# Kernel tuning notes

Measured on AMD Instinct MI355X. Metric: run time of the kernel, lower is better.

## Reference

```python
import jax, jax.numpy as jnp
import numpy as np
import jax.scipy.linalg

BATCH = 1048576
M_NUM = 2
DT = 0.0166667
NN_RATIO = 0.5
SLOPE = 0.01  # torch LeakyReLU default negative_slope


def setup_inputs() -> dict:
    key = jax.random.key(0)
    ks = jax.random.split(key, 16)
    inp = {}
    inp["SS"] = jax.random.normal(ks[0], (BATCH, 2), dtype=jnp.float32)
    inp["Alphas"] = jax.random.uniform(ks[1], (BATCH, M_NUM), dtype=jnp.float32)
    # per-muscle scalar parameters (positive so sqrt(K*I) is valid)
    inp["K0s"] = jax.random.uniform(ks[2], (M_NUM,), minval=0.5, maxval=1.5)
    inp["K1s"] = jax.random.uniform(ks[3], (M_NUM,), minval=0.5, maxval=1.5)
    inp["L0s"] = jax.random.uniform(ks[4], (M_NUM,), minval=0.5, maxval=1.5)
    inp["L1s"] = jax.random.uniform(ks[5], (M_NUM,), minval=0.1, maxval=0.6)
    inp["Ms"] = jnp.array([1.0, -1.0], dtype=jnp.float32)  # moment arms
    inp["I_p"] = jnp.array([1.0], dtype=jnp.float32)
    inp["B_p"] = jnp.array([0.05], dtype=jnp.float32)
    inp["K_p"] = jnp.array([1.0], dtype=jnp.float32)
    # per-muscle compensational MLP weights: 3-32-32-32-1 (eval mode, dropout off)
    s = 0.1
    inp["W1"] = jax.random.normal(ks[6], (M_NUM, 3, 32)) * s
    inp["b1"] = jax.random.normal(ks[7], (M_NUM, 32)) * s
    inp["W2"] = jax.random.normal(ks[8], (M_NUM, 32, 32)) * s
    inp["b2"] = jax.random.normal(ks[9], (M_NUM, 32)) * s
    inp["W3"] = jax.random.normal(ks[10], (M_NUM, 32, 32)) * s
    inp["b3"] = jax.random.normal(ks[11], (M_NUM, 32)) * s
    inp["W4"] = jax.random.normal(ks[12], (M_NUM, 32, 1)) * s
    inp["b4"] = jax.random.normal(ks[13], (M_NUM, 1)) * s
    return inp


def _leaky(x):
    return jnp.where(x >= 0, x, SLOPE * x)


def reference(SS, Alphas, K0s, K1s, L0s, L1s, Ms, I_p, B_p, K_p,
              W1, b1, W2, b2, W3, b3, W4, b4):
    B = SS.shape[0]
    a = jnp.clip(Alphas, 0.0, 1.0)                      # (B, m)
    # muscle length / speed via scalar moment arms
    l = SS[:, 0:1] * Ms[None, :]                        # (B, m)
    dl = SS[:, 1:2] * Ms[None, :]                       # (B, m)
    # compensational MLPs, vectorized over muscles
    x = jnp.stack([l, dl, a], axis=-1)                  # (B, m, 3)
    h = _leaky(jnp.einsum('bmi,mio->bmo', x, W1) + b1[None])
    h = _leaky(jnp.einsum('bmi,mio->bmo', h, W2) + b2[None])
    h = _leaky(jnp.einsum('bmi,mio->bmo', h, W3) + b3[None])
    nn_out = jnp.tanh(jnp.einsum('bmi,mio->bmo', h, W4) + b4[None])[..., 0] * NN_RATIO  # (B, m)

    I0, B0p, K0p = I_p[0], B_p[0], K_p[0]
    K_m = K0s[None, :] + K1s[None, :] * a               # (B, m)
    K_tot = jnp.sum(K_m * Ms[None, :] ** 2, axis=1)     # (B,)
    A10 = -(K_tot + K0p) / I0
    D = 2.0 * jnp.sqrt(K_tot * I0)
    A11 = -(D + B0p) / I0
    B_F = K_m * (L0s[None, :] + L1s[None, :] * a - jnp.abs(l)) \
        + K1s[None, :] * L1s[None, :] * a * a * nn_out   # (B, m)
    B10 = jnp.sum(B_F * Ms[None, :], axis=1) / I0       # (B,)

    # Build block matrix M6 = [[A*dt, B*dt, 0], [0, 0, I2], [0, 0, 0]]
    M6 = jnp.zeros((B, 6, 6), dtype=SS.dtype)
    M6 = M6.at[:, 0, 1].set(DT)
    M6 = M6.at[:, 1, 0].set(A10 * DT)
    M6 = M6.at[:, 1, 1].set(A11 * DT)
    M6 = M6.at[:, 1, 2].set(B10 * DT)
    M6 = M6.at[:, 1, 3].set(DT / I0)
    M6 = M6.at[:, 2, 4].set(1.0)
    M6 = M6.at[:, 3, 5].set(1.0)

    expMT = jax.vmap(jax.scipy.linalg.expm)(M6)         # (B, 6, 6)
    Ad = expMT[:, :2, :2]
    Bd1 = expMT[:, :2, 4:6]
    Bd0 = expMT[:, :2, 2:4] - Bd1
    u = jnp.array([1.0, 0.0], dtype=SS.dtype)           # U0 = U1 = [1, 0]
    SSout = (jnp.einsum('bij,bj->bi', Ad, SS)
             + jnp.einsum('bij,j->bi', Bd0, u)
             + jnp.einsum('bij,j->bi', Bd1, u))          # (B, 2)
    return SSout[:, :1], SSout
```

## Files before the change

kernel.cpp:

```cpp
#include <hip/hip_runtime.h>
#include <hip/hip_bf16.h>

#define NTHREADS 256
#define WAVES    4
#define GPW      4
#define DT_F     0.0166667f

typedef _Float16 f16x8 __attribute__((ext_vector_type(8)));
typedef _Float16 f16x4 __attribute__((ext_vector_type(4)));
typedef _Float16 f16x2 __attribute__((ext_vector_type(2)));
typedef float    f32x4 __attribute__((ext_vector_type(4)));

#define BF16_PROBE 0xBF803F80u

#define OW1 0
#define OB1 192
#define OW2 256
#define OB2 2368
#define OW3 2432
#define OB3 4544
#define OW4 4608
#define OB4 4672
#define SMEM_F 4680

__device__ __forceinline__ float leaky(float x) { return fmaxf(x, 0.01f * x); }

__device__ __forceinline__ float tanh_fast(float x) {
    const float xc = fminf(fmaxf(x, -10.0f), 10.0f);
    const float t  = __expf(2.0f * xc);
    return (t - 1.0f) * __builtin_amdgcn_rcpf(t + 1.0f);
}

__device__ __forceinline__ f16x2 pkrtz(float a, float b) {
    return __builtin_bit_cast(f16x2, __builtin_amdgcn_cvt_pkrtz(a, b));
}

__device__ __forceinline__ f16x4 leaky_cvt(const f32x4 D) {
    f16x2 lo = pkrtz(D[0], D[1]);
    f16x2 hi = pkrtz(D[2], D[3]);
    const f16x2 sl = {(_Float16)0.01f, (_Float16)0.01f};
    lo = __builtin_elementwise_max(lo, lo * sl);
    hi = __builtin_elementwise_max(hi, hi * sl);
    return __builtin_shufflevector(lo, hi, 0, 1, 2, 3);
}

__device__ __forceinline__ f16x8 concat8(const f16x4 a, const f16x4 b) {
    return __builtin_shufflevector(a, b, 0, 1, 2, 3, 4, 5, 6, 7);
}

__device__ __forceinline__ void epilogue_math(
    const float* P, float ss0, float ss1, float a0, float a1,
    float nn0, float nn1, float& o0f, float& o1f)
{
    const float K00 = P[0], K01 = P[1], K10 = P[2], K11 = P[3];
    const float L00 = P[4], L01 = P[5], L10 = P[6], L11 = P[7];
    const float Ms0 = P[8], Ms1 = P[9];
    const float I0  = P[10], B0p = P[11], K0p = P[12];

    const float Km0   = fmaf(K10, a0, K00);
    const float Km1   = fmaf(K11, a1, K01);
    const float K_tot = Km0*Ms0*Ms0 + Km1*Ms1*Ms1;
    const float invI  = 1.0f / I0;
    const float A10   = -(K_tot + K0p) * invI;
    const float Dd    = 2.0f * sqrtf(K_tot * I0);
    const float A11   = -(Dd + B0p) * invI;
    const float absl0 = fabsf(ss0 * Ms0);
    const float absl1 = fabsf(ss0 * Ms1);
    const float BF0   = Km0 * (L00 + L10*a0 - absl0) + K10*L10*a0*a0*nn0;
    const float BF1   = Km1 * (L01 + L11*a1 - absl1) + K11*L11*a1*a1*nn1;
    const float B10   = (BF0*Ms0 + BF1*Ms1) * invI;

    const float t01 = DT_F;
    const float t10 = A10 * DT_F;
    const float t11 = A11 * DT_F;

    float p00 = 1.0f/120.0f, p01 = 0.0f, p10 = 0.0f, p11 = 1.0f/120.0f;
    const float coef[4] = {1.0f/24.0f, 1.0f/6.0f, 0.5f, 1.0f};
    #pragma unroll
    for (int j = 0; j < 4; ++j) {
        const float cj  = coef[j];
        const float n00 = p01*t10 + cj;
        const float n01 = p00*t01 + p01*t11;
        const float n10 = p11*t10;
        const float n11 = p10*t01 + p11*t11 + cj;
        p00 = n00; p01 = n01; p10 = n10; p11 = n11;
    }
    const float e00 = 1.0f + t01*p10;
    const float e01 = t01*p11;
    const float e10 = t10*p00 + t11*p10;
    const float e11 = 1.0f + t10*p01 + t11*p11;

    const float cscale = DT_F * B10;
    o0f = fmaf(e00, ss0, fmaf(e01, ss1, p01 * cscale));
    o1f = fmaf(e10, ss0, fmaf(e11, ss1, p11 * cscale));
}

__device__ __forceinline__ float ldb(const __hip_bfloat16* p, int i) {
    return __bfloat162float(p[i]);
}

__device__ void run_bf16_fallback(
    const void* SSv, const void* ALv, const void* K0sv, const void* K1sv,
    const void* L0sv, const void* L1sv, const void* Msv, const void* I_pv,
    const void* B_pv, const void* K_pv, const void* W1v, const void* b1v,
    const void* W2v, const void* b2v, const void* W3v, const void* b3v,
    const void* W4v, const void* b4v, void* outv, int batch)
{
    const __hip_bfloat16* SS = (const __hip_bfloat16*)SSv;
    const __hip_bfloat16* AL = (const __hip_bfloat16*)ALv;
    const __hip_bfloat16* W1 = (const __hip_bfloat16*)W1v;
    const __hip_bfloat16* b1 = (const __hip_bfloat16*)b1v;
    const __hip_bfloat16* W2 = (const __hip_bfloat16*)W2v;
    const __hip_bfloat16* b2 = (const __hip_bfloat16*)b2v;
    const __hip_bfloat16* W3 = (const __hip_bfloat16*)W3v;
    const __hip_bfloat16* b3 = (const __hip_bfloat16*)b3v;
    const __hip_bfloat16* W4 = (const __hip_bfloat16*)W4v;
    const __hip_bfloat16* b4 = (const __hip_bfloat16*)b4v;

    float P[13];
    P[0] = ldb((const __hip_bfloat16*)K0sv, 0); P[1] = ldb((const __hip_bfloat16*)K0sv, 1);
    P[2] = ldb((const __hip_bfloat16*)K1sv, 0); P[3] = ldb((const __hip_bfloat16*)K1sv, 1);
    P[4] = ldb((const __hip_bfloat16*)L0sv, 0); P[5] = ldb((const __hip_bfloat16*)L0sv, 1);
    P[6] = ldb((const __hip_bfloat16*)L1sv, 0); P[7] = ldb((const __hip_bfloat16*)L1sv, 1);
    P[8] = ldb((const __hip_bfloat16*)Msv, 0);  P[9] = ldb((const __hip_bfloat16*)Msv, 1);
    P[10] = ldb((const __hip_bfloat16*)I_pv, 0);
    P[11] = ldb((const __hip_bfloat16*)B_pv, 0);
    P[12] = ldb((const __hip_bfloat16*)K_pv, 0);

    const int stride = gridDim.x * blockDim.x;
    for (int e = blockIdx.x * blockDim.x + threadIdx.x; e < batch; e += stride) {
        const float ss0 = ldb(SS, 2*e), ss1 = ldb(SS, 2*e+1);
        float a0 = fminf(fmaxf(ldb(AL, 2*e),   0.0f), 1.0f);
        float a1 = fminf(fmaxf(ldb(AL, 2*e+1), 0.0f), 1.0f);
        float nn[2];
        #pragma unroll 1
        for (int m = 0; m < 2; ++m) {
            const float am = m ? a1 : a0;
            const float l = ss0 * P[8+m], dl = ss1 * P[8+m];
            float h[32];
            #pragma unroll
            for (int o = 0; o < 32; ++o)
                h[o] = leaky(fmaf(l, ldb(W1, m*96+o),
                             fmaf(dl, ldb(W1, m*96+32+o),
                             fmaf(am, ldb(W1, m*96+64+o), ldb(b1, m*32+o)))));
            float g[32];
            #pragma unroll 1
            for (int oc = 0; oc < 4; ++oc) {
                float acc[8];
                #pragma unroll
                for (int j = 0; j < 8; ++j) acc[j] = ldb(b2, m*32+oc*8+j);
                #pragma unroll
                for (int k = 0; k < 32; ++k) {
                    #pragma unroll
                    for (int j = 0; j < 8; ++j)
                        acc[j] = fmaf(h[k], ldb(W2, m*1024+k*32+oc*8+j), acc[j]);
                }
                #pragma unroll
                for (int j = 0; j < 8; ++j) g[oc*8+j] = leaky(acc[j]);
            }
            float h3[32];
            #pragma unroll 1
            for (int oc = 0; oc < 4; ++oc) {
                float acc[8];
                #pragma unroll
                for (int j = 0; j < 8; ++j) acc[j] = ldb(b3, m*32+oc*8+j);
                #pragma unroll
                for (int k = 0; k < 32; ++k) {
                    #pragma unroll
                    for (int j = 0; j < 8; ++j)
                        acc[j] = fmaf(g[k], ldb(W3, m*1024+k*32+oc*8+j), acc[j]);
                }
                #pragma unroll
                for (int j = 0; j < 8; ++j) h3[oc*8+j] = leaky(acc[j]);
            }
            float acc = ldb(b4, m);
            #pragma unroll
            for (int k = 0; k < 32; ++k) acc = fmaf(h3[k], ldb(W4, m*32+k), acc);
            nn[m] = tanh_fast(acc) * 0.5f;
        }
        float o0f, o1f;
        epilogue_math(P, ss0, ss1, a0, a1, nn[0], nn[1], o0f, o1f);
        __hip_bfloat16* out0 = (__hip_bfloat16*)outv;
        __hip_bfloat162* out1 = (__hip_bfloat162*)(out0 + batch);
        out0[e] = __float2bfloat16(o0f);
        __hip_bfloat162 pr;
        pr.x = __float2bfloat16(o0f);
        pr.y = __float2bfloat16(o1f);
        out1[e] = pr;
    }
}

__global__ __launch_bounds__(NTHREADS) void joint_kernel(
    const void* __restrict__ SSv, const void* __restrict__ ALv,
    const void* __restrict__ K0sv, const void* __restrict__ K1sv,
    const void* __restrict__ L0sv, const void* __restrict__ L1sv,
    const void* __restrict__ Msv,  const void* __restrict__ I_pv,
    const void* __restrict__ B_pv, const void* __restrict__ K_pv,
    const void* __restrict__ W1v,  const void* __restrict__ b1v,
    const void* __restrict__ W2v,  const void* __restrict__ b2v,
    const void* __restrict__ W3v,  const void* __restrict__ b3v,
    const void* __restrict__ W4v,  const void* __restrict__ b4v,
    void* __restrict__ outv, int batch)
{
    const unsigned probe = *(const unsigned*)Msv;
    if (probe == BF16_PROBE) {
        run_bf16_fallback(SSv, ALv, K0sv, K1sv, L0sv, L1sv, Msv, I_pv, B_pv,
                          K_pv, W1v, b1v, W2v, b2v, W3v, b3v, W4v, b4v,
                          outv, batch);
        return;
    }

    const float* SS = (const float*)SSv;
    const float* AL = (const float*)ALv;
    const float* W1 = (const float*)W1v;  const float* b1 = (const float*)b1v;
    const float* W2 = (const float*)W2v;  const float* b2 = (const float*)b2v;
    const float* W3 = (const float*)W3v;  const float* b3 = (const float*)b3v;
    const float* W4 = (const float*)W4v;  const float* b4 = (const float*)b4v;

    const int tid  = threadIdx.x;
    const int wave = tid >> 6;
    const int lane = tid & 63;
    const int n    = lane & 15;
    const int q    = lane >> 4;
    const int gh0  = ((n >> 2) << 3) + (n & 3);

    __shared__ __align__(16) float sm[SMEM_F];
    for (int i = tid; i < 192;  i += NTHREADS) sm[OW1+i] = W1[i];
    for (int i = tid; i < 2048; i += NTHREADS) {
        const int mi = i >> 10, rem = i & 1023, in = rem >> 5, out = rem & 31;
        sm[OW2 + mi*1056 + in*33 + out] = W2[i];
        sm[OW3 + mi*1056 + in*33 + out] = W3[i];
    }
    for (int i = tid; i < 64;   i += NTHREADS) {
        sm[OB1+i] = b1[i]; sm[OB2+i] = b2[i];
        sm[OB3+i] = b3[i]; sm[OW4+i] = W4[i];
    }
    if (tid < 2) sm[OB4+tid] = b4[tid];
    __syncthreads();

    f16x4 A1[2][2];
    #pragma unroll
    for (int mi = 0; mi < 2; ++mi)
        #pragma unroll
        for (int h = 0; h < 2; ++h)
            #pragma unroll
            for (int j = 0; j < 4; ++j) {
                const int k = q*4 + j;
                const int g = gh0 + h*4;
                float v = 0.0f;
                if (k < 3)       v = sm[OW1 + mi*96 + k*32 + g];
                else if (k == 3) v = sm[OB1 + mi*32 + g];
                A1[mi][h][j] = (_Float16)v;
            }
    f16x8 A2[2][2], A3[2][2];
    #pragma unroll
    for (int mi = 0; mi < 2; ++mi)
        #pragma unroll
        for (int h = 0; h < 2; ++h) {
            const int g = gh0 + h*4;
            #pragma unroll
            for (int j = 0; j < 8; ++j) {
                const int in = q*8 + j;
                A2[mi][h][j] = (_Float16)sm[OW2 + mi*1056 + in*33 + g];
                A3[mi][h][j] = (_Float16)sm[OW3 + mi*1056 + in*33 + g];
            }
        }
    f16x8 A4[2];
    #pragma unroll
    for (int mi = 0; mi < 2; ++mi)
        #pragma unroll
        for (int j = 0; j < 8; ++j)
            A4[mi][j] = (_Float16)sm[OW4 + mi*32 + q*8 + j];
    f32x4 Cb2[2][2], Cb3[2][2];
    #pragma unroll
    for (int mi = 0; mi < 2; ++mi)
        #pragma unroll
        for (int h = 0; h < 2; ++h) {
            Cb2[mi][h] = *(const f32x4*)&sm[OB2 + mi*32 + q*8 + h*4];
            Cb3[mi][h] = *(const f32x4*)&sm[OB3 + mi*32 + q*8 + h*4];
        }
    const float b4s0 = sm[OB4], b4s1 = sm[OB4+1];

    float P[13];
    P[0]  = ((const float*)K0sv)[0]; P[1]  = ((const float*)K0sv)[1];
    P[2]  = ((const float*)K1sv)[0]; P[3]  = ((const float*)K1sv)[1];
    P[4]  = ((const float*)L0sv)[0]; P[5]  = ((const float*)L0sv)[1];
    P[6]  = ((const float*)L1sv)[0]; P[7]  = ((const float*)L1sv)[1];
    P[8]  = ((const float*)Msv)[0];  P[9]  = ((const float*)Msv)[1];
    P[10] = ((const float*)I_pv)[0];
    P[11] = ((const float*)B_pv)[0];
    P[12] = ((const float*)K_pv)[0];

    const f32x4 zero = {0.0f, 0.0f, 0.0f, 0.0f};
    const int groupBase = (blockIdx.x * WAVES + wave) * GPW;

    #pragma unroll 1
    for (int g = 0; g < GPW; ++g) {
        const int ebase = (groupBase + g) * 64;
        float my_r0 = 0.0f, my_r1 = 0.0f;

        #pragma unroll 1
        for (int p = 0; p < 2; ++p) {
            float2 s[2];
            float a0c[2], a1c[2];
            #pragma unroll
            for (int ti = 0; ti < 2; ++ti) {
                const int e  = ebase + (2*p + ti)*16 + n;
                const int eg = min(e, batch - 1);
                s[ti] = ((const float2*)SS)[eg];
                const float2 al = ((const float2*)AL)[eg];
                a0c[ti] = fminf(fmaxf(al.x, 0.0f), 1.0f);
                a1c[ti] = fminf(fmaxf(al.y, 0.0f), 1.0f);
            }

            f16x4 B1[2][2];
            #pragma unroll
            for (int ti = 0; ti < 2; ++ti)
                #pragma unroll
                for (int mi = 0; mi < 2; ++mi) {
                    const float Msm = P[8 + mi];
                    const float am  = mi ? a1c[ti] : a0c[ti];
                    const f16x2 blo = pkrtz(s[ti].x * Msm, s[ti].y * Msm);
                    const f16x2 bhi = pkrtz(am, 1.0f);
                    B1[ti][mi] = __builtin_shufflevector(blo, bhi, 0, 1, 2, 3);
                }

            f32x4 D[2][2][2];
            #pragma unroll
            for (int ti = 0; ti < 2; ++ti)
                #pragma unroll
                for (int mi = 0; mi < 2; ++mi) {
                    D[ti][mi][0] = __builtin_amdgcn_mfma_f32_16x16x16f16(A1[mi][0], B1[ti][mi], zero, 0, 0, 0);
                    D[ti][mi][1] = __builtin_amdgcn_mfma_f32_16x16x16f16(A1[mi][1], B1[ti][mi], zero, 0, 0, 0);
                }
            f16x8 Bx[2][2];
            #pragma unroll
            for (int ti = 0; ti < 2; ++ti)
                #pragma unroll
                for (int mi = 0; mi < 2; ++mi)
                    Bx[ti][mi] = concat8(leaky_cvt(D[ti][mi][0]), leaky_cvt(D[ti][mi][1]));

            #pragma unroll
            for (int ti = 0; ti < 2; ++ti)
                #pragma unroll
                for (int mi = 0; mi < 2; ++mi) {
                    D[ti][mi][0] = __builtin_amdgcn_mfma_f32_16x16x32_f16(A2[mi][0], Bx[ti][mi], Cb2[mi][0], 0, 0, 0);
                    D[ti][mi][1] = __builtin_amdgcn_mfma_f32_16x16x32_f16(A2[mi][1], Bx[ti][mi], Cb2[mi][1], 0, 0, 0);
                }
            #pragma unroll
            for (int ti = 0; ti < 2; ++ti)
                #pragma unroll
                for (int mi = 0; mi < 2; ++mi)
                    Bx[ti][mi] = concat8(leaky_cvt(D[ti][mi][0]), leaky_cvt(D[ti][mi][1]));

            #pragma unroll
            for (int ti = 0; ti < 2; ++ti)
                #pragma unroll
                for (int mi = 0; mi < 2; ++mi) {
                    D[ti][mi][0] = __builtin_amdgcn_mfma_f32_16x16x32_f16(A3[mi][0], Bx[ti][mi], Cb3[mi][0], 0, 0, 0);
                    D[ti][mi][1] = __builtin_amdgcn_mfma_f32_16x16x32_f16(A3[mi][1], Bx[ti][mi], Cb3[mi][1], 0, 0, 0);
                }
            #pragma unroll
            for (int ti = 0; ti < 2; ++ti)
                #pragma unroll
                for (int mi = 0; mi < 2; ++mi)
                    Bx[ti][mi] = concat8(leaky_cvt(D[ti][mi][0]), leaky_cvt(D[ti][mi][1]));

            #pragma unroll
            for (int ti = 0; ti < 2; ++ti) {
                const bool own = (q == (2*p + ti));
                #pragma unroll
                for (int mi = 0; mi < 2; ++mi) {
                    f32x4 G = __builtin_amdgcn_mfma_f32_16x16x32_f16(A4[mi], Bx[ti][mi], zero, 0, 0, 0);
                    const float r = G[0] + (mi ? b4s1 : b4s0);
                    if (mi == 0) my_r0 = own ? r : my_r0;
                    else         my_r1 = own ? r : my_r1;
                }
            }
        }

        const int eo  = ebase + lane;
        const int eog = min(eo, batch - 1);
        const float2 se  = ((const float2*)SS)[eog];
        const float2 ale = ((const float2*)AL)[eog];
        const float a0 = fminf(fmaxf(ale.x, 0.0f), 1.0f);
        const float a1 = fminf(fmaxf(ale.y, 0.0f), 1.0f);
        const float nn0 = tanh_fast(my_r0) * 0.5f;
        const float nn1 = tanh_fast(my_r1) * 0.5f;
        float o0f, o1f;
        epilogue_math(P, se.x, se.y, a0, a1, nn0, nn1, o0f, o1f);
        if (eo < batch) {
            ((float*)outv)[eo] = o0f;
            ((float2*)((float*)outv + batch))[eo] = make_float2(o0f, o1f);
        }
    }
}

extern "C" void kernel_launch(void* const* d_in, const int* in_sizes, int n_in,
                              void* d_out, int out_size, void* d_ws, size_t ws_size,
                              hipStream_t stream) {
    const int batch = in_sizes[0] / 2;
    const int elemsPerBlock = 64 * GPW * WAVES;
    const int grid = (batch + elemsPerBlock - 1) / elemsPerBlock;
    joint_kernel<<<grid, NTHREADS, 0, stream>>>(
        d_in[0], d_in[1], d_in[2], d_in[3], d_in[4], d_in[5], d_in[6],
        d_in[7], d_in[8], d_in[9], d_in[10], d_in[11], d_in[12], d_in[13],
        d_in[14], d_in[15], d_in[16], d_in[17], d_out, batch);
}
```

Before: 126.8 us.

## Process all four column tiles per group at once and simplify 2x2 expm epilogue

The per-group loop over two half-groups of two 16-column tiles is replaced by one pass over all four tiles. Each MFMA layer stage now issues twice as many independent instructions, which gives more room to hide MFMA latency. The epilogue's 2x2 Taylor/Horner matrix exponential is reduced to a two-scalar recurrence that exploits the fixed t00=0 structure, cutting ALU work. Launch bounds now declare one block per SM so the larger register footprint fits, at the risk of lower occupancy.

Result: slower. 131.1 us (+3.3%).

```diff
diff --git a/kernel.cpp b/kernel.cpp
--- a/kernel.cpp
+++ b/kernel.cpp
@@ -73,26 +73,22 @@
     const float t01 = DT_F;
     const float t10 = A10 * DT_F;
     const float t11 = A11 * DT_F;
-
-    float p00 = 1.0f/120.0f, p01 = 0.0f, p10 = 0.0f, p11 = 1.0f/120.0f;
+    const float u   = t01 * t10;
+
+    float a = 1.0f/120.0f, b = 0.0f;
     const float coef[4] = {1.0f/24.0f, 1.0f/6.0f, 0.5f, 1.0f};
     #pragma unroll
     for (int j = 0; j < 4; ++j) {
-        const float cj  = coef[j];
-        const float n00 = p01*t10 + cj;
-        const float n01 = p00*t01 + p01*t11;
-        const float n10 = p11*t10;
-        const float n11 = p10*t01 + p11*t11 + cj;
-        p00 = n00; p01 = n01; p10 = n10; p11 = n11;
-    }
-    const float e00 = 1.0f + t01*p10;
-    const float e01 = t01*p11;
-    const float e10 = t10*p00 + t11*p10;
-    const float e11 = 1.0f + t10*p01 + t11*p11;
-
-    const float cscale = DT_F * B10;
-    o0f = fmaf(e00, ss0, fmaf(e01, ss1, p01 * cscale));
-    o1f = fmaf(e10, ss0, fmaf(e11, ss1, p11 * cscale));
+        const float an = fmaf(b, u, coef[j]);
+        const float bn = fmaf(b, t11, a);
+        a = an; b = bn;
+    }
+    const float c   = fmaf(b, t11, a);
+    const float e00 = fmaf(b, u, 1.0f);
+    const float cs  = DT_F * B10;
+
+    o0f = fmaf(e00, ss0, fmaf(c * t01, ss1, cs * (b * t01)));
+    o1f = fmaf(c * t10, ss0, fmaf(fmaf(c, t11, e00), ss1, cs * c));
 }
 
 __device__ __forceinline__ float ldb(const __hip_bfloat16* p, int i) {
@@ -190,7 +186,7 @@
     }
 }
 
-__global__ __launch_bounds__(NTHREADS) void joint_kernel(
+__global__ __launch_bounds__(NTHREADS, 1) void joint_kernel(
     const void* __restrict__ SSv, const void* __restrict__ ALv,
     const void* __restrict__ K0sv, const void* __restrict__ K1sv,
     const void* __restrict__ L0sv, const void* __restrict__ L1sv,
@@ -297,85 +293,82 @@
     #pragma unroll 1
     for (int g = 0; g < GPW; ++g) {
         const int ebase = (groupBase + g) * 64;
+
+        float2 s[4];
+        float a0c[4], a1c[4];
+        #pragma unroll
+        for (int t = 0; t < 4; ++t) {
+            const int e  = ebase + t*16 + n;
+            const int eg = min(e, batch - 1);
+            s[t] = ((const float2*)SS)[eg];
+            const float2 al = ((const float2*)AL)[eg];
+            a0c[t] = fminf(fmaxf(al.x, 0.0f), 1.0f);
+            a1c[t] = fminf(fmaxf(al.y, 0.0f), 1.0f);
+        }
+
+        f16x4 B1[4][2];
+        #pragma unroll
+        for (int t = 0; t < 4; ++t)
+            #pragma unroll
+            for (int mi = 0; mi < 2; ++mi) {
+                const float Msm = P[8 + mi];
+                const float am  = mi ? a1c[t] : a0c[t];
+                const f16x2 blo = pkrtz(s[t].x * Msm, s[t].y * Msm);
+                const f16x2 bhi = pkrtz(am, 1.0f);
+                B1[t][mi] = __builtin_shufflevector(blo, bhi, 0, 1, 2, 3);
+            }
+
+        f32x4 D[4][2][2];
+        #pragma unroll
+        for (int t = 0; t < 4; ++t)
+            #pragma unroll
+            for (int mi = 0; mi < 2; ++mi) {
+                D[t][mi][0] = __builtin_amdgcn_mfma_f32_16x16x16f16(A1[mi][0], B1[t][mi], zero, 0, 0, 0);
+                D[t][mi][1] = __builtin_amdgcn_mfma_f32_16x16x16f16(A1[mi][1], B1[t][mi], zero, 0, 0, 0);
+            }
+        f16x8 Bx[4][2];
+        #pragma unroll
+        for (int t = 0; t < 4; ++t)
+            #pragma unroll
+            for (int mi = 0; mi < 2; ++mi)
+                Bx[t][mi] = concat8(leaky_cvt(D[t][mi][0]), leaky_cvt(D[t][mi][1]));
+
+        #pragma unroll
+        for (int t = 0; t < 4; ++t)
+            #pragma unroll
+            for (int mi = 0; mi < 2; ++mi) {
+                D[t][mi][0] = __builtin_amdgcn_mfma_f32_16x16x32_f16(A2[mi][0], Bx[t][mi], Cb2[mi][0], 0, 0, 0);
+                D[t][mi][1] = __builtin_amdgcn_mfma_f32_16x16x32_f16(A2[mi][1], Bx[t][mi], Cb2[mi][1], 0, 0, 0);
+            }
+        #pragma unroll
+        for (int t = 0; t < 4; ++t)
+            #pragma unroll
+            for (int mi = 0; mi < 2; ++mi)
+                Bx[t][mi] = concat8(leaky_cvt(D[t][mi][0]), leaky_cvt(D[t][mi][1]));
+
+        #pragma unroll
+        for (int t = 0; t < 4; ++t)
+            #pragma unroll
+            for (int mi = 0; mi < 2; ++mi) {
+                D[t][mi][0] = __builtin_amdgcn_mfma_f32_16x16x32_f16(A3[mi][0], Bx[t][mi], Cb3[mi][0], 0, 0, 0);
+                D[t][mi][1] = __builtin_amdgcn_mfma_f32_16x16x32_f16(A3[mi][1], Bx[t][mi], Cb3[mi][1], 0, 0, 0);
+            }
+        #pragma unroll
+        for (int t = 0; t < 4; ++t)
+            #pragma unroll
+            for (int mi = 0; mi < 2; ++mi)
+                Bx[t][mi] = concat8(leaky_cvt(D[t][mi][0]), leaky_cvt(D[t][mi][1]));
+
         float my_r0 = 0.0f, my_r1 = 0.0f;
-
-        #pragma unroll 1
-        for (int p = 0; p < 2; ++p) {
-            float2 s[2];
-            float a0c[2], a1c[2];
-            #pragma unroll
-            for (int ti = 0; ti < 2; ++ti) {
-                const int e  = ebase + (2*p + ti)*16 + n;
-                const int eg = min(e, batch - 1);
-                s[ti] = ((const float2*)SS)[eg];
-                const float2 al = ((const float2*)AL)[eg];
-                a0c[ti] = fminf(fmaxf(al.x, 0.0f), 1.0f);
-                a1c[ti] = fminf(fmaxf(al.y, 0.0f), 1.0f);
-            }
-
-            f16x4 B1[2][2];
-            #pragma unroll
-            for (int ti = 0; ti < 2; ++ti)
-                #pragma unroll
-                for (int mi = 0; mi < 2; ++mi) {
-                    const float Msm = P[8 + mi];
-                    const float am  = mi ? a1c[ti] : a0c[ti];
-                    const f16x2 blo = pkrtz(s[ti].x * Msm, s[ti].y * Msm);
-                    const f16x2 bhi = pkrtz(am, 1.0f);
-                    B1[ti][mi] = __builtin_shufflevector(blo, bhi, 0, 1, 2, 3);
-                }
-
-            f32x4 D[2][2][2];
-            #pragma unroll
-            for (int ti = 0; ti < 2; ++ti)
-                #pragma unroll
-                for (int mi = 0; mi < 2; ++mi) {
-                    D[ti][mi][0] = __builtin_amdgcn_mfma_f32_16x16x16f16(A1[mi][0], B1[ti][mi], zero, 0, 0, 0);
-                    D[ti][mi][1] = __builtin_amdgcn_mfma_f32_16x16x16f16(A1[mi][1], B1[ti][mi], zero, 0, 0, 0);
-                }
-            f16x8 Bx[2][2];
-            #pragma unroll
-            for (int ti = 0; ti < 2; ++ti)
-                #pragma unroll
-                for (int mi = 0; mi < 2; ++mi)
-                    Bx[ti][mi] = concat8(leaky_cvt(D[ti][mi][0]), leaky_cvt(D[ti][mi][1]));
-
-            #pragma unroll
-            for (int ti = 0; ti < 2; ++ti)
-                #pragma unroll
-                for (int mi = 0; mi < 2; ++mi) {
-                    D[ti][mi][0] = __builtin_amdgcn_mfma_f32_16x16x32_f16(A2[mi][0], Bx[ti][mi], Cb2[mi][0], 0, 0, 0);
-                    D[ti][mi][1] = __builtin_amdgcn_mfma_f32_16x16x32_f16(A2[mi][1], Bx[ti][mi], Cb2[mi][1], 0, 0, 0);
-                }
-            #pragma unroll
-            for (int ti = 0; ti < 2; ++ti)
-                #pragma unroll
-                for (int mi = 0; mi < 2; ++mi)
-                    Bx[ti][mi] = concat8(leaky_cvt(D[ti][mi][0]), leaky_cvt(D[ti][mi][1]));
-
-            #pragma unroll
-            for (int ti = 0; ti < 2; ++ti)
-                #pragma unroll
-                for (int mi = 0; mi < 2; ++mi) {
-                    D[ti][mi][0] = __builtin_amdgcn_mfma_f32_16x16x32_f16(A3[mi][0], Bx[ti][mi], Cb3[mi][0], 0, 0, 0);
-                    D[ti][mi][1] = __builtin_amdgcn_mfma_f32_16x16x32_f16(A3[mi][1], Bx[ti][mi], Cb3[mi][1], 0, 0, 0);
-                }
-            #pragma unroll
-            for (int ti = 0; ti < 2; ++ti)
-                #pragma unroll
-                for (int mi = 0; mi < 2; ++mi)
-                    Bx[ti][mi] = concat8(leaky_cvt(D[ti][mi][0]), leaky_cvt(D[ti][mi][1]));
-
-            #pragma unroll
-            for (int ti = 0; ti < 2; ++ti) {
-                const bool own = (q == (2*p + ti));
-                #pragma unroll
-                for (int mi = 0; mi < 2; ++mi) {
-                    f32x4 G = __builtin_amdgcn_mfma_f32_16x16x32_f16(A4[mi], Bx[ti][mi], zero, 0, 0, 0);
-                    const float r = G[0] + (mi ? b4s1 : b4s0);
-                    if (mi == 0) my_r0 = own ? r : my_r0;
-                    else         my_r1 = own ? r : my_r1;
-                }
+        #pragma unroll
+        for (int t = 0; t < 4; ++t) {
+            const bool own = (q == t);
+            #pragma unroll
+            for (int mi = 0; mi < 2; ++mi) {
+                f32x4 G = __builtin_amdgcn_mfma_f32_16x16x32_f16(A4[mi], Bx[t][mi], zero, 0, 0, 0);
+                const float r = G[0] + (mi ? b4s1 : b4s0);
+                if (mi == 0) my_r0 = own ? r : my_r0;
+                else         my_r1 = own ? r : my_r1;
             }
         }
 
```
